# Performance work log

Measured on AMD Instinct MI355X. Metric: run time of the kernel, lower is better.

## Reference

```python
import jax, jax.numpy as jnp
import numpy as np

N, T, H, W, C = 4, 8, 64, 64, 512
WS = 8  # window size; H, W are exact multiples so pad/depad are identity


def setup_inputs() -> dict:
    key = jax.random.key(0)
    k1, k2, k3, k4 = jax.random.split(key, 4)
    x = jax.random.normal(k1, (N, T, H, W, C), dtype=jnp.float32)
    local_pos_embed = jax.random.normal(k2, (WS, WS, C), dtype=jnp.float32)
    W_in = jax.random.normal(k3, (3 * C, C), dtype=jnp.float32) * 0.02
    b_in = jnp.zeros((3 * C,), dtype=jnp.float32)
    W_out = jax.random.normal(k4, (C, C), dtype=jnp.float32) * 0.02
    b_out = jnp.zeros((C,), dtype=jnp.float32)
    return {"x": x, "local_pos_embed": local_pos_embed, "W_in": W_in,
            "b_in": b_in, "W_out": W_out, "b_out": b_out, "num_heads": 8}


def reference(x, local_pos_embed, W_in, b_in, W_out, b_out, num_heads):
    n, t, h, w, c = x.shape
    ws = local_pos_embed.shape[0]
    nh, nw = h // ws, w // ws
    head_dim = c // num_heads
    scale = 1.0 / jnp.sqrt(jnp.asarray(head_dim, dtype=x.dtype))

    # window partition: (N*T, H, W, C) -> (N*T*nh*nw, ws*ws, C)
    xw = x.reshape(n * t, nh, ws, nw, ws, c)
    xw = xw.transpose(0, 1, 3, 2, 4, 5).reshape(n * t * nh * nw, ws * ws, c)

    pos = local_pos_embed.reshape(ws * ws, c)  # flatten(0,1)
    qk_in = xw + pos[None, :, :]               # pos added to q,k only

    Wq, Wk, Wv = W_in[:c], W_in[c:2 * c], W_in[2 * c:]
    bq, bk, bv = b_in[:c], b_in[c:2 * c], b_in[2 * c:]

    B, S = qk_in.shape[0], qk_in.shape[1]
    q = (qk_in @ Wq.T + bq).reshape(B, S, num_heads, head_dim)
    k = (qk_in @ Wk.T + bk).reshape(B, S, num_heads, head_dim)
    v = (xw @ Wv.T + bv).reshape(B, S, num_heads, head_dim)

    scores = jnp.einsum('bqhd,bkhd->bhqk', q * scale, k)
    attn = jax.nn.softmax(scores, axis=-1)
    out = jnp.einsum('bhqk,bkhd->bqhd', attn, v).reshape(B, S, c)
    out = out @ W_out.T + b_out

    # reverse window partition
    out = out.reshape(n * t, nh, nw, ws, ws, c)
    out = out.transpose(0, 1, 3, 2, 4, 5).reshape(n, t, h, w, c)
    return out
```

## Files before the change

### kernel.cpp

```cpp
#include <hip/hip_runtime.h>

typedef _Float16 f16;
typedef unsigned int u32;
typedef f16 f16x8 __attribute__((ext_vector_type(8)));
typedef f16 f16x4 __attribute__((ext_vector_type(4)));
typedef float f32x4 __attribute__((ext_vector_type(4)));


__device__ __forceinline__ int src_row(int m) {
    int win = m >> 6, s = m & 63;
    return ((win >> 6) << 12) | (((win >> 3) & 7) << 9) | ((s >> 3) << 6) |
           ((win & 7) << 3) | (s & 7);
}

__device__ __forceinline__ void gload_lds16(const void* g, void* lds) {
    __builtin_amdgcn_global_load_lds(
        (const __attribute__((address_space(1))) u32*)g,
        (__attribute__((address_space(3))) u32*)lds, 16, 0, 0);
}

__global__ __launch_bounds__(256) void prep_weights_k(
        const float* __restrict__ Wi, const float* __restrict__ Wo,
        f16* __restrict__ Wi_h, f16* __restrict__ Wo_h) {
    int i = blockIdx.x * 256 + threadIdx.x;
    const float4* src;
    f16* dst;
    int idx;
    if (i < 196608) { src = (const float4*)Wi; dst = Wi_h; idx = i; }
    else            { src = (const float4*)Wo; dst = Wo_h; idx = i - 196608; }
    float4 v = src[idx];
    f16x4 h = {(f16)v.x, (f16)v.y, (f16)v.z, (f16)v.w};
    *(f16x4*)(dst + (size_t)idx * 4) = h;
}

__global__ __launch_bounds__(256) void prep_bias_k(
        const float* __restrict__ pos, const float* __restrict__ Wi,
        const float* __restrict__ b_in, float* __restrict__ biasT) {
    int idx = blockIdx.x * 256 + threadIdx.x;
    int s = idx / 1536, o = idx % 1536;
    float acc = b_in[o];
    if (o < 1024) {
        const float4* p4 = (const float4*)(pos + (size_t)s * 512);
        const float4* w4 = (const float4*)(Wi + (size_t)o * 512);
        #pragma unroll 4
        for (int c = 0; c < 128; ++c) {
            float4 a = p4[c], b = w4[c];
            acc += a.x * b.x + a.y * b.y + a.z * b.z + a.w * b.w;
        }
    }
    biasT[idx] = acc;
}

__global__ __launch_bounds__(256) void prep_x_k(
        const float* __restrict__ x, f16* __restrict__ xh, int m0) {
    int i = blockIdx.x * 256 + threadIdx.x;
    int ml = i >> 6, c8 = (i & 63) * 8;
    int sr = src_row(m0 + ml);
    const float4* s4 = (const float4*)(x + (size_t)sr * 512 + c8);
    float4 a = s4[0], b = s4[1];
    f16x8 hv = {(f16)a.x, (f16)a.y, (f16)a.z, (f16)a.w,
                (f16)b.x, (f16)b.y, (f16)b.z, (f16)b.w};
    *(f16x8*)(xh + (size_t)ml * 512 + c8) = hv;
}

__global__ void __launch_bounds__(512, 2) qkv_gemm8_k(
        const f16* __restrict__ xh, const f16* __restrict__ Wh,
        const float* __restrict__ biasT, f16* __restrict__ qk,
        f16* __restrict__ vT, int nblk) {
    extern __shared__ f16 lds[];
    int tid = threadIdx.x;
    int lane = tid & 63, wid = tid >> 6;
    int l15 = lane & 15, g = lane >> 4;
    int wm = wid >> 2, wn = wid & 3;
    int sid = (blockIdx.x & 7) * (nblk >> 3) + (blockIdx.x >> 3);
    int bm = sid / 6, bn = sid % 6;
    const f16* Ap = xh + (size_t)bm * 256 * 512;
    const f16* Bp = Wh + (size_t)bn * 256 * 512;

    int li0 = tid, li1 = tid + 512;
    int r0 = li0 >> 3, c0 = li0 & 7, r1 = li1 >> 3, c1 = li1 & 7;
    int off0 = r0 * 512 + ((c0 ^ (r0 & 7)) * 8);
    int off1 = r1 * 512 + ((c1 ^ (r1 & 7)) * 8);

    auto stage = [&](const f16* panel, int ldsbase, int tt, int h) {
        int tb = tt & 1;
        int dst = ldsbase + (tb * 2 + h) * 8192 + wid * 512;
        const f16* src = panel + h * 65536 + tt * 64;
        gload_lds16(src + off0, (void*)&lds[dst]);
        gload_lds16(src + off1, (void*)&lds[dst + 4096]);
    };

    f32x4 acc[8][4];
    f32x4 zero4 = {0.f, 0.f, 0.f, 0.f};
    #pragma unroll
    for (int a = 0; a < 8; ++a)
        #pragma unroll
        for (int b = 0; b < 4; ++b) acc[a][b] = zero4;
    f16x8 bf[4][2];

    stage(Ap, 0, 0, 0); stage(Ap, 0, 0, 1);
    stage(Bp, 32768, 0, 0); stage(Bp, 32768, 0, 1);
    stage(Ap, 0, 1, 0); stage(Ap, 0, 1, 1);
    stage(Bp, 32768, 1, 0); stage(Bp, 32768, 1, 1);
    asm volatile("s_waitcnt vmcnt(8)" ::: "memory");
    __builtin_amdgcn_s_barrier();

    #pragma unroll
    for (int tt = 0; tt < 8; ++tt) {
        int tb = tt & 1;
        const f16* Ab = &lds[(tb * 2 + wm) * 8192];
        const f16* Bb = &lds[32768 + (tb * 2 + (wn >> 1)) * 8192];
        #pragma unroll
        for (int q = 0; q < 4; ++q) {
            f16x8 af[2][2];
            #pragma unroll
            for (int ml = 0; ml < 2; ++ml) {
                int rr = (q * 2 + ml) * 16 + l15;
                #pragma unroll
                for (int ks = 0; ks < 2; ++ks)
                    af[ml][ks] = *(const f16x8*)&Ab[rr * 64 + (((ks * 4 + g) ^ (rr & 7)) * 8)];
            }
            if (q == 0) {
                #pragma unroll
                for (int nf = 0; nf < 4; ++nf) {
                    int rb = (wn & 1) * 64 + nf * 16 + l15;
                    #pragma unroll
                    for (int ks = 0; ks < 2; ++ks)
                        bf[nf][ks] = *(const f16x8*)&Bb[rb * 64 + (((ks * 4 + g) ^ (rb & 7)) * 8)];
                }
            }
            if (q <= 1) {
                if ((tt & 1) ? (tt + 1 < 8) : (tt >= 2)) stage(Ap, 0, tt + 1, q);
            } else {
                if (tt + 2 < 8) stage(Bp, 32768, tt + 2, q - 2);
            }
            __builtin_amdgcn_s_barrier();
            __builtin_amdgcn_s_setprio(1);
            #pragma unroll
            for (int ml = 0; ml < 2; ++ml)
                #pragma unroll
                for (int nf = 0; nf < 4; ++nf)
                    #pragma unroll
                    for (int ks = 0; ks < 2; ++ks)
                        acc[q * 2 + ml][nf] = __builtin_amdgcn_mfma_f32_16x16x32_f16(
                            af[ml][ks], bf[nf][ks], acc[q * 2 + ml][nf], 0, 0, 0);
            __builtin_amdgcn_s_setprio(0);
            if (q == 3) {
                if (tt < 6)       asm volatile("s_waitcnt vmcnt(4)" ::: "memory");
                else if (tt == 6) asm volatile("s_waitcnt vmcnt(0)" ::: "memory");
            }
            __builtin_amdgcn_s_barrier();
        }
    }

    int browg = bm * 256 + wm * 128;
    if (bn < 4) {
        #pragma unroll
        for (int half = 0; half < 2; ++half) {
            if (wm == half) {
                #pragma unroll
                for (int mf = 0; mf < 8; ++mf) {
                    #pragma unroll
                    for (int nf = 0; nf < 4; ++nf) {
                        int col = bn * 256 + wn * 64 + nf * 16 + l15;
                        int cloc = wn * 64 + nf * 16 + l15;
                        #pragma unroll
                        for (int j = 0; j < 4; ++j) {
                            int r = mf * 16 + g * 4 + j;
                            float v = acc[mf][nf][j] + biasT[(r & 63) * 1536 + col];
                            *(f16*)((char*)lds + r * 512 + ((cloc * 2) ^ ((r & 7) << 4))) = (f16)v;
                        }
                    }
                }
            }
            __syncthreads();
            int rowg0 = bm * 256 + half * 128;
            #pragma unroll
            for (int i = 0; i < 8; ++i) {
                int c = i * 512 + tid;
                int r = c >> 5, seg = c & 31;
                f16x8 v = *(const f16x8*)((char*)lds + r * 512 + ((seg * 16) ^ ((r & 7) << 4)));
                *(f16x8*)(qk + (size_t)(rowg0 + r) * 1024 + bn * 256 + seg * 8) = v;
            }
            __syncthreads();
        }
    } else {
        __syncthreads();
        char* T = (char*)lds;
        int bn2 = bn - 4;
        #pragma unroll
        for (int mf = 0; mf < 8; ++mf) {
            #pragma unroll
            for (int nf = 0; nf < 4; ++nf) {
                int dl = wn * 64 + nf * 16 + l15;
                float bo = biasT[1024 + bn2 * 256 + dl];
                #pragma unroll
                for (int j = 0; j < 4; ++j) {
                    int sl = wm * 128 + mf * 16 + g * 4 + j;
                    *(f16*)(T + dl * 512 + ((sl * 2) ^ ((dl & 7) << 4))) =
                        (f16)(acc[mf][nf][j] + bo);
                }
            }
        }
        __syncthreads();
        #pragma unroll
        for (int r = 0; r < 16; ++r) {
            int c = r * 512 + tid;
            int dl = c >> 5, s0 = (c & 31) * 8;
            f16x8 v = *(const f16x8*)(T + dl * 512 + ((s0 * 2) ^ ((dl & 7) << 4)));
            int gcol = bn2 * 256 + dl;
            int head = gcol >> 6, dd = gcol & 63;
            int win = bm * 4 + (s0 >> 6);
            *(f16x8*)(vT + (size_t)win * 32768 + head * 4096 + dd * 64 + (s0 & 63)) = v;
        }
    }
}

__global__ __launch_bounds__(512) void attn_k(
        const f16* __restrict__ qk, const f16* __restrict__ vT,
        f16* __restrict__ attn_h) {
    __shared__ __align__(16) char S[64 * 1024];
    int tid = threadIdx.x;
    int lane = tid & 63, h = tid >> 6;
    int l15 = lane & 15, g = lane >> 4;
    const f16* baseqk = qk + (size_t)blockIdx.x * 65536;
    const f16* basev  = vT + (size_t)blockIdx.x * 32768 + h * 4096;
    int qc = h * 64, kc = 512 + h * 64;

    f32x4 zero4 = {0.f, 0.f, 0.f, 0.f};
    f32x4 acc[4][4];
    #pragma unroll
    for (int a = 0; a < 4; ++a)
        #pragma unroll
        for (int b = 0; b < 4; ++b) acc[a][b] = zero4;

    {
        f16x8 qf[4][2], kf[4][2];
        #pragma unroll
        for (int mf = 0; mf < 4; ++mf)
            #pragma unroll
            for (int ks = 0; ks < 2; ++ks)
                qf[mf][ks] = *reinterpret_cast<const f16x8*>(baseqk + (size_t)(mf * 16 + l15) * 1024 + qc + ks * 32 + g * 8);
        #pragma unroll
        for (int nf = 0; nf < 4; ++nf)
            #pragma unroll
            for (int ks = 0; ks < 2; ++ks)
                kf[nf][ks] = *reinterpret_cast<const f16x8*>(baseqk + (size_t)(nf * 16 + l15) * 1024 + kc + ks * 32 + g * 8);
        #pragma unroll
        for (int ks = 0; ks < 2; ++ks)
            #pragma unroll
            for (int ki = 0; ki < 4; ++ki)
                #pragma unroll
                for (int qi = 0; qi < 4; ++qi)
                    acc[ki][qi] = __builtin_amdgcn_mfma_f32_16x16x32_f16(kf[ki][ks], qf[qi][ks], acc[ki][qi], 0, 0, 0);
    }

    f16x8 vf[4][2];
    #pragma unroll
    for (int nf = 0; nf < 4; ++nf)
        #pragma unroll
        for (int ks = 0; ks < 2; ++ks)
            vf[nf][ks] = *reinterpret_cast<const f16x8*>(basev + (nf * 16 + l15) * 64 + ks * 32 + g * 8);

    char* Sh = S + h * 8192;
    #pragma unroll
    for (int qi = 0; qi < 4; ++qi) {
        float mx = -1e30f;
        #pragma unroll
        for (int ki = 0; ki < 4; ++ki)
            #pragma unroll
            for (int j = 0; j < 4; ++j) mx = fmaxf(mx, acc[ki][qi][j]);
        mx = fmaxf(mx, __shfl_xor(mx, 16));
        mx = fmaxf(mx, __shfl_xor(mx, 32));
        float sum = 0.f;
        #pragma unroll
        for (int ki = 0; ki < 4; ++ki)
            #pragma unroll
            for (int j = 0; j < 4; ++j) {
                float e = __expf((acc[ki][qi][j] - mx) * 0.125f);
                acc[ki][qi][j] = e;
                sum += e;
            }
        sum += __shfl_xor(sum, 16);
        sum += __shfl_xor(sum, 32);
        float rinv = __fdividef(1.0f, sum);
        int qrow = qi * 16 + l15;
        char* rowp = Sh + qrow * 128;
        int sw = (qrow & 7) << 4;
        #pragma unroll
        for (int ki = 0; ki < 4; ++ki)
            #pragma unroll
            for (int j = 0; j < 4; ++j)
                *(f16*)(rowp + (((ki * 16 + g * 4 + j) * 2) ^ sw)) = (f16)(acc[ki][qi][j] * rinv);
    }

    f32x4 acc2[4][4];
    #pragma unroll
    for (int a = 0; a < 4; ++a)
        #pragma unroll
        for (int b = 0; b < 4; ++b) acc2[a][b] = zero4;
    #pragma unroll
    for (int ks = 0; ks < 2; ++ks)
        #pragma unroll
        for (int mf = 0; mf < 4; ++mf) {
            int rr = mf * 16 + l15;
            f16x8 pa = *reinterpret_cast<const f16x8*>(Sh + rr * 128 + (((ks * 32 + g * 8) * 2) ^ ((rr & 7) << 4)));
            #pragma unroll
            for (int nf = 0; nf < 4; ++nf)
                acc2[mf][nf] = __builtin_amdgcn_mfma_f32_16x16x32_f16(pa, vf[nf][ks], acc2[mf][nf], 0, 0, 0);
        }

    #pragma unroll
    for (int mf = 0; mf < 4; ++mf)
        #pragma unroll
        for (int nf = 0; nf < 4; ++nf)
            #pragma unroll
            for (int j = 0; j < 4; ++j) {
                int r = mf * 16 + g * 4 + j;
                *(f16*)(Sh + r * 128 + (((nf * 16 + l15) * 2) ^ ((r & 7) << 4))) = (f16)acc2[mf][nf][j];
            }
    __syncthreads();
    f16* dst = attn_h + (size_t)blockIdx.x * 32768;
    #pragma unroll
    for (int i = 0; i < 8; ++i) {
        int c = i * 512 + tid;
        int row = c >> 6, seg = c & 63;
        f16x8 v = *(const f16x8*)(S + (seg >> 3) * 8192 + row * 128 + (((seg & 7) * 16) ^ ((row & 7) << 4)));
        *(f16x8*)(dst + row * 512 + seg * 8) = v;
    }
}

__global__ void __launch_bounds__(512, 2) proj_gemm8_k(
        const f16* __restrict__ attn_h, const f16* __restrict__ Woh,
        const float* __restrict__ b_out, float* __restrict__ out, int nblk, int m0) {
    extern __shared__ f16 lds[];
    int tid = threadIdx.x;
    int lane = tid & 63, wid = tid >> 6;
    int l15 = lane & 15, g = lane >> 4;
    int wm = wid >> 2, wn = wid & 3;
    int sid = (blockIdx.x & 7) * (nblk >> 3) + (blockIdx.x >> 3);
    int bm = sid >> 1, bn = sid & 1;
    const f16* Ap = attn_h + (size_t)bm * 256 * 512;
    const f16* Bp = Woh + (size_t)bn * 256 * 512;

    int li0 = tid, li1 = tid + 512;
    int r0 = li0 >> 3, c0 = li0 & 7, r1 = li1 >> 3, c1 = li1 & 7;
    int off0 = r0 * 512 + ((c0 ^ (r0 & 7)) * 8);
    int off1 = r1 * 512 + ((c1 ^ (r1 & 7)) * 8);

    auto stage = [&](const f16* panel, int ldsbase, int tt, int h) {
        int tb = tt & 1;
        int dst = ldsbase + (tb * 2 + h) * 8192 + wid * 512;
        const f16* src = panel + h * 65536 + tt * 64;
        gload_lds16(src + off0, (void*)&lds[dst]);
        gload_lds16(src + off1, (void*)&lds[dst + 4096]);
    };

    f32x4 acc[8][4];
    f32x4 zero4 = {0.f, 0.f, 0.f, 0.f};
    #pragma unroll
    for (int a = 0; a < 8; ++a)
        #pragma unroll
        for (int b = 0; b < 4; ++b) acc[a][b] = zero4;
    f16x8 bf[4][2];

    stage(Ap, 0, 0, 0); stage(Ap, 0, 0, 1);
    stage(Bp, 32768, 0, 0); stage(Bp, 32768, 0, 1);
    stage(Ap, 0, 1, 0); stage(Ap, 0, 1, 1);
    stage(Bp, 32768, 1, 0); stage(Bp, 32768, 1, 1);
    asm volatile("s_waitcnt vmcnt(8)" ::: "memory");
    __builtin_amdgcn_s_barrier();

    #pragma unroll
    for (int tt = 0; tt < 8; ++tt) {
        int tb = tt & 1;
        const f16* Ab = &lds[(tb * 2 + wm) * 8192];
        const f16* Bb = &lds[32768 + (tb * 2 + (wn >> 1)) * 8192];
        #pragma unroll
        for (int q = 0; q < 4; ++q) {
            f16x8 af[2][2];
            #pragma unroll
            for (int ml = 0; ml < 2; ++ml) {
                int rr = (q * 2 + ml) * 16 + l15;
                #pragma unroll
                for (int ks = 0; ks < 2; ++ks)
                    af[ml][ks] = *(const f16x8*)&Ab[rr * 64 + (((ks * 4 + g) ^ (rr & 7)) * 8)];
            }
            if (q == 0) {
                #pragma unroll
                for (int nf = 0; nf < 4; ++nf) {
                    int rb = (wn & 1) * 64 + nf * 16 + l15;
                    #pragma unroll
                    for (int ks = 0; ks < 2; ++ks)
                        bf[nf][ks] = *(const f16x8*)&Bb[rb * 64 + (((ks * 4 + g) ^ (rb & 7)) * 8)];
                }
            }
            if (q <= 1) {
                if ((tt & 1) ? (tt + 1 < 8) : (tt >= 2)) stage(Ap, 0, tt + 1, q);
            } else {
                if (tt + 2 < 8) stage(Bp, 32768, tt + 2, q - 2);
            }
            __builtin_amdgcn_s_barrier();
            __builtin_amdgcn_s_setprio(1);
            #pragma unroll
            for (int ml = 0; ml < 2; ++ml)
                #pragma unroll
                for (int nf = 0; nf < 4; ++nf)
                    #pragma unroll
                    for (int ks = 0; ks < 2; ++ks)
                        acc[q * 2 + ml][nf] = __builtin_amdgcn_mfma_f32_16x16x32_f16(
                            af[ml][ks], bf[nf][ks], acc[q * 2 + ml][nf], 0, 0, 0);
            __builtin_amdgcn_s_setprio(0);
            if (q == 3) {
                if (tt < 6)       asm volatile("s_waitcnt vmcnt(4)" ::: "memory");
                else if (tt == 6) asm volatile("s_waitcnt vmcnt(0)" ::: "memory");
            }
            __builtin_amdgcn_s_barrier();
        }
    }

    int browg = bm * 256 + wm * 128, bcolg = bn * 256 + wn * 64;
    #pragma unroll
    for (int nf = 0; nf < 4; ++nf) {
        int col = bcolg + nf * 16 + l15;
        float bo = b_out[col];
        #pragma unroll
        for (int mf = 0; mf < 8; ++mf) {
            #pragma unroll
            for (int j = 0; j < 4; ++j) {
                int srow = src_row(m0 + browg + mf * 16 + g * 4 + j);
                out[(size_t)srow * 512 + col] = acc[mf][nf][j] + bo;
            }
        }
    }
}

extern "C" void kernel_launch(void* const* d_in, const int* in_sizes, int n_in,
                              void* d_out, int out_size, void* d_ws, size_t ws_size,
                              hipStream_t stream) {
    (void)in_sizes; (void)n_in; (void)out_size;
    const float* x     = (const float*)d_in[0];
    const float* pos   = (const float*)d_in[1];
    const float* W_in  = (const float*)d_in[2];
    const float* b_in  = (const float*)d_in[3];
    const float* W_out = (const float*)d_in[4];
    const float* b_out = (const float*)d_in[5];
    float* out = (float*)d_out;

    char* ws = (char*)d_ws;
    f16*   Wi_h  = (f16*)ws;
    f16*   Wo_h  = (f16*)(ws + 1572864);
    float* biasT = (float*)(ws + 2097152);
    const size_t fixed = 2490368;

    int chunks = 1;
    while (chunks < 64) {
        size_t need = fixed + ((size_t)131072 / chunks) * 4096;
        if (need <= ws_size) break;
        chunks <<= 1;
    }
    int Mc = 131072 / chunks;
    f16* xh = (f16*)(ws + fixed);
    f16* qk = (f16*)(ws + fixed + (size_t)Mc * 1024);
    f16* vT = (f16*)(ws + fixed + (size_t)Mc * 3072);
    int nblk  = (Mc / 256) * 6;
    int nblk2 = (Mc / 256) * 2;

    static_cast<void>(hipFuncSetAttribute((const void*)qkv_gemm8_k,
        hipFuncAttributeMaxDynamicSharedMemorySize, 131072));
    static_cast<void>(hipFuncSetAttribute((const void*)proj_gemm8_k,
        hipFuncAttributeMaxDynamicSharedMemorySize, 131072));

    prep_weights_k<<<1024, 256, 0, stream>>>(W_in, W_out, Wi_h, Wo_h);
    prep_bias_k<<<384, 256, 0, stream>>>(pos, W_in, b_in, biasT);
    for (int c = 0; c < chunks; ++c) {
        int m0 = c * Mc;
        prep_x_k<<<Mc / 4, 256, 0, stream>>>(x, xh, m0);
        qkv_gemm8_k<<<nblk, 512, 131072, stream>>>(xh, Wi_h, biasT, qk, vT, nblk);
        attn_k<<<Mc / 64, 512, 0, stream>>>(qk, vT, xh);
        proj_gemm8_k<<<nblk2, 512, 131072, stream>>>(xh, Wo_h, b_out, out, nblk2, m0);
    }
}
```

Measured before the change: 603.4 us.

## Make GEMM blocks process four M tiles with a continuous cross-tile prefetch pipeline

Both the QKV and projection GEMM kernels now handle four consecutive 256-row tiles per block, keeping the LDS prefetch pipeline running across tile boundaries instead of refilling it for each tile. This amortises prologue and epilogue latency and cuts the grid to a quarter of its previous size. The QKV epilogue also drops its LDS-staged transpose and writes q/k and vT straight to global memory with scalar or 4-wide stores. In exchange the grid may be too small to fill all CUs, and the direct stores are less coalesced than the staged 16-byte ones.

```diff
diff --git a/kernel.cpp b/kernel.cpp
--- a/kernel.cpp
+++ b/kernel.cpp
@@ -73,8 +73,8 @@
     int l15 = lane & 15, g = lane >> 4;
     int wm = wid >> 2, wn = wid & 3;
     int sid = (blockIdx.x & 7) * (nblk >> 3) + (blockIdx.x >> 3);
-    int bm = sid / 6, bn = sid % 6;
-    const f16* Ap = xh + (size_t)bm * 256 * 512;
+    int bmg = sid / 6, bn = sid % 6;
+    const f16* Ap = xh + (size_t)bmg * 4 * 256 * 512;
     const f16* Bp = Wh + (size_t)bn * 256 * 512;
 
     int li0 = tid, li1 = tid + 512;
@@ -82,13 +82,18 @@
     int off0 = r0 * 512 + ((c0 ^ (r0 & 7)) * 8);
     int off1 = r1 * 512 + ((c1 ^ (r1 & 7)) * 8);
 
-    auto stage = [&](const f16* panel, int ldsbase, int tt, int h) {
-        int tb = tt & 1;
-        int dst = ldsbase + (tb * 2 + h) * 8192 + wid * 512;
-        const f16* src = panel + h * 65536 + tt * 64;
+    auto stageA = [&](int Tabs, int h) {
+        int dst = ((Tabs & 1) * 2 + h) * 8192 + wid * 512;
+        const f16* src = Ap + (size_t)(Tabs >> 3) * 131072 + h * 65536 + (Tabs & 7) * 64;
         gload_lds16(src + off0, (void*)&lds[dst]);
         gload_lds16(src + off1, (void*)&lds[dst + 4096]);
     };
+    auto stageB = [&](int Tabs, int h) {
+        int dst = 32768 + ((Tabs & 1) * 2 + h) * 8192 + wid * 512;
+        const f16* src = Bp + h * 65536 + (Tabs & 7) * 64;
+        gload_lds16(src + off0, (void*)&lds[dst]);
+        gload_lds16(src + off1, (void*)&lds[dst + 4096]);
+    };
 
     f32x4 acc[8][4];
     f32x4 zero4 = {0.f, 0.f, 0.f, 0.f};
@@ -98,121 +103,103 @@
         for (int b = 0; b < 4; ++b) acc[a][b] = zero4;
     f16x8 bf[4][2];
 
-    stage(Ap, 0, 0, 0); stage(Ap, 0, 0, 1);
-    stage(Bp, 32768, 0, 0); stage(Bp, 32768, 0, 1);
-    stage(Ap, 0, 1, 0); stage(Ap, 0, 1, 1);
-    stage(Bp, 32768, 1, 0); stage(Bp, 32768, 1, 1);
+    stageA(0, 0); stageA(0, 1); stageB(0, 0); stageB(0, 1);
+    stageA(1, 0); stageA(1, 1); stageB(1, 0); stageB(1, 1);
     asm volatile("s_waitcnt vmcnt(8)" ::: "memory");
     __builtin_amdgcn_s_barrier();
 
-    #pragma unroll
-    for (int tt = 0; tt < 8; ++tt) {
-        int tb = tt & 1;
-        const f16* Ab = &lds[(tb * 2 + wm) * 8192];
-        const f16* Bb = &lds[32768 + (tb * 2 + (wn >> 1)) * 8192];
-        #pragma unroll
-        for (int q = 0; q < 4; ++q) {
-            f16x8 af[2][2];
-            #pragma unroll
-            for (int ml = 0; ml < 2; ++ml) {
-                int rr = (q * 2 + ml) * 16 + l15;
-                #pragma unroll
-                for (int ks = 0; ks < 2; ++ks)
-                    af[ml][ks] = *(const f16x8*)&Ab[rr * 64 + (((ks * 4 + g) ^ (rr & 7)) * 8)];
-            }
-            if (q == 0) {
+    for (int p = 0; p < 4; ++p) {
+        #pragma unroll
+        for (int tt = 0; tt < 8; ++tt) {
+            const f16* Ab = &lds[((tt & 1) * 2 + wm) * 8192];
+            const f16* Bb = &lds[32768 + ((tt & 1) * 2 + (wn >> 1)) * 8192];
+            #pragma unroll
+            for (int q = 0; q < 4; ++q) {
+                f16x8 af[2][2];
+                #pragma unroll
+                for (int ml = 0; ml < 2; ++ml) {
+                    int rr = (q * 2 + ml) * 16 + l15;
+                    #pragma unroll
+                    for (int ks = 0; ks < 2; ++ks)
+                        af[ml][ks] = *(const f16x8*)&Ab[rr * 64 + (((ks * 4 + g) ^ (rr & 7)) * 8)];
+                }
+                if (q == 0) {
+                    #pragma unroll
+                    for (int nf = 0; nf < 4; ++nf) {
+                        int rb = (wn & 1) * 64 + nf * 16 + l15;
+                        #pragma unroll
+                        for (int ks = 0; ks < 2; ++ks)
+                            bf[nf][ks] = *(const f16x8*)&Bb[rb * 64 + (((ks * 4 + g) ^ (rb & 7)) * 8)];
+                    }
+                }
+                if (q <= 1) {
+                    bool doA = (tt >= 1 || p > 0) && (tt < 7 || p < 3);
+                    if (doA) stageA(p * 8 + tt + 1, q);
+                } else {
+                    bool doB = (tt < 6 || p < 3);
+                    if (doB) stageB(p * 8 + tt + 2, q - 2);
+                }
+                __builtin_amdgcn_s_barrier();
+                __builtin_amdgcn_s_setprio(1);
+                #pragma unroll
+                for (int ml = 0; ml < 2; ++ml)
+                    #pragma unroll
+                    for (int nf = 0; nf < 4; ++nf)
+                        #pragma unroll
+                        for (int ks = 0; ks < 2; ++ks)
+                            acc[q * 2 + ml][nf] = __builtin_amdgcn_mfma_f32_16x16x32_f16(
+                                af[ml][ks], bf[nf][ks], acc[q * 2 + ml][nf], 0, 0, 0);
+                __builtin_amdgcn_s_setprio(0);
+                if (q == 3) {
+                    if (tt < 6) {
+                        asm volatile("s_waitcnt vmcnt(4)" ::: "memory");
+                    } else if (tt == 6) {
+                        if (p < 3) asm volatile("s_waitcnt vmcnt(4)" ::: "memory");
+                        else       asm volatile("s_waitcnt vmcnt(0)" ::: "memory");
+                    } else {
+                        if (p < 3) asm volatile("s_waitcnt vmcnt(4)" ::: "memory");
+                    }
+                }
+                __builtin_amdgcn_s_barrier();
+            }
+        }
+
+        int browg = (bmg * 4 + p) * 256 + wm * 128;
+        if (bn < 4) {
+            #pragma unroll
+            for (int mf = 0; mf < 8; ++mf) {
                 #pragma unroll
                 for (int nf = 0; nf < 4; ++nf) {
-                    int rb = (wn & 1) * 64 + nf * 16 + l15;
-                    #pragma unroll
-                    for (int ks = 0; ks < 2; ++ks)
-                        bf[nf][ks] = *(const f16x8*)&Bb[rb * 64 + (((ks * 4 + g) ^ (rb & 7)) * 8)];
-                }
-            }
-            if (q <= 1) {
-                if ((tt & 1) ? (tt + 1 < 8) : (tt >= 2)) stage(Ap, 0, tt + 1, q);
-            } else {
-                if (tt + 2 < 8) stage(Bp, 32768, tt + 2, q - 2);
-            }
-            __builtin_amdgcn_s_barrier();
-            __builtin_amdgcn_s_setprio(1);
-            #pragma unroll
-            for (int ml = 0; ml < 2; ++ml)
-                #pragma unroll
-                for (int nf = 0; nf < 4; ++nf)
-                    #pragma unroll
-                    for (int ks = 0; ks < 2; ++ks)
-                        acc[q * 2 + ml][nf] = __builtin_amdgcn_mfma_f32_16x16x32_f16(
-                            af[ml][ks], bf[nf][ks], acc[q * 2 + ml][nf], 0, 0, 0);
-            __builtin_amdgcn_s_setprio(0);
-            if (q == 3) {
-                if (tt < 6)       asm volatile("s_waitcnt vmcnt(4)" ::: "memory");
-                else if (tt == 6) asm volatile("s_waitcnt vmcnt(0)" ::: "memory");
-            }
-            __builtin_amdgcn_s_barrier();
-        }
-    }
-
-    int browg = bm * 256 + wm * 128;
-    if (bn < 4) {
-        #pragma unroll
-        for (int half = 0; half < 2; ++half) {
-            if (wm == half) {
-                #pragma unroll
-                for (int mf = 0; mf < 8; ++mf) {
-                    #pragma unroll
-                    for (int nf = 0; nf < 4; ++nf) {
-                        int col = bn * 256 + wn * 64 + nf * 16 + l15;
-                        int cloc = wn * 64 + nf * 16 + l15;
-                        #pragma unroll
-                        for (int j = 0; j < 4; ++j) {
-                            int r = mf * 16 + g * 4 + j;
-                            float v = acc[mf][nf][j] + biasT[(r & 63) * 1536 + col];
-                            *(f16*)((char*)lds + r * 512 + ((cloc * 2) ^ ((r & 7) << 4))) = (f16)v;
-                        }
+                    int col = bn * 256 + wn * 64 + nf * 16 + l15;
+                    #pragma unroll
+                    for (int j = 0; j < 4; ++j) {
+                        int row = browg + mf * 16 + g * 4 + j;
+                        float v = acc[mf][nf][j] + biasT[(row & 63) * 1536 + col];
+                        qk[(size_t)row * 1024 + col] = (f16)v;
                     }
                 }
             }
-            __syncthreads();
-            int rowg0 = bm * 256 + half * 128;
-            #pragma unroll
-            for (int i = 0; i < 8; ++i) {
-                int c = i * 512 + tid;
-                int r = c >> 5, seg = c & 31;
-                f16x8 v = *(const f16x8*)((char*)lds + r * 512 + ((seg * 16) ^ ((r & 7) << 4)));
-                *(f16x8*)(qk + (size_t)(rowg0 + r) * 1024 + bn * 256 + seg * 8) = v;
-            }
-            __syncthreads();
-        }
-    } else {
-        __syncthreads();
-        char* T = (char*)lds;
-        int bn2 = bn - 4;
-        #pragma unroll
-        for (int mf = 0; mf < 8; ++mf) {
-            #pragma unroll
-            for (int nf = 0; nf < 4; ++nf) {
-                int dl = wn * 64 + nf * 16 + l15;
-                float bo = biasT[1024 + bn2 * 256 + dl];
-                #pragma unroll
-                for (int j = 0; j < 4; ++j) {
-                    int sl = wm * 128 + mf * 16 + g * 4 + j;
-                    *(f16*)(T + dl * 512 + ((sl * 2) ^ ((dl & 7) << 4))) =
-                        (f16)(acc[mf][nf][j] + bo);
-                }
-            }
-        }
-        __syncthreads();
-        #pragma unroll
-        for (int r = 0; r < 16; ++r) {
-            int c = r * 512 + tid;
-            int dl = c >> 5, s0 = (c & 31) * 8;
-            f16x8 v = *(const f16x8*)(T + dl * 512 + ((s0 * 2) ^ ((dl & 7) << 4)));
-            int gcol = bn2 * 256 + dl;
-            int head = gcol >> 6, dd = gcol & 63;
-            int win = bm * 4 + (s0 >> 6);
-            *(f16x8*)(vT + (size_t)win * 32768 + head * 4096 + dd * 64 + (s0 & 63)) = v;
-        }
+        } else {
+            int bn2 = bn - 4;
+            #pragma unroll
+            for (int mf = 0; mf < 8; ++mf) {
+                int sl = browg + mf * 16 + g * 4;
+                int win = sl >> 6, s = sl & 63;
+                #pragma unroll
+                for (int nf = 0; nf < 4; ++nf) {
+                    int dl = bn2 * 256 + wn * 64 + nf * 16 + l15;
+                    float bo = biasT[1024 + dl];
+                    int head = dl >> 6, dd = dl & 63;
+                    f16x4 v = {(f16)(acc[mf][nf][0] + bo), (f16)(acc[mf][nf][1] + bo),
+                               (f16)(acc[mf][nf][2] + bo), (f16)(acc[mf][nf][3] + bo)};
+                    *(f16x4*)(vT + (size_t)win * 32768 + head * 4096 + dd * 64 + s) = v;
+                }
+            }
+        }
+        #pragma unroll
+        for (int a = 0; a < 8; ++a)
+            #pragma unroll
+            for (int b = 0; b < 4; ++b) acc[a][b] = zero4;
     }
 }
 
@@ -339,8 +326,8 @@
     int l15 = lane & 15, g = lane >> 4;
     int wm = wid >> 2, wn = wid & 3;
     int sid = (blockIdx.x & 7) * (nblk >> 3) + (blockIdx.x >> 3);
-    int bm = sid >> 1, bn = sid & 1;
-    const f16* Ap = attn_h + (size_t)bm * 256 * 512;
+    int bmg = sid >> 1, bn = sid & 1;
+    const f16* Ap = attn_h + (size_t)bmg * 4 * 256 * 512;
     const f16* Bp = Woh + (size_t)bn * 256 * 512;
 
     int li0 = tid, li1 = tid + 512;
@@ -348,13 +335,18 @@
     int off0 = r0 * 512 + ((c0 ^ (r0 & 7)) * 8);
     int off1 = r1 * 512 + ((c1 ^ (r1 & 7)) * 8);
 
-    auto stage = [&](const f16* panel, int ldsbase, int tt, int h) {
-        int tb = tt & 1;
-        int dst = ldsbase + (tb * 2 + h) * 8192 + wid * 512;
-        const f16* src = panel + h * 65536 + tt * 64;
+    auto stageA = [&](int Tabs, int h) {
+        int dst = ((Tabs & 1) * 2 + h) * 8192 + wid * 512;
+        const f16* src = Ap + (size_t)(Tabs >> 3) * 131072 + h * 65536 + (Tabs & 7) * 64;
         gload_lds16(src + off0, (void*)&lds[dst]);
         gload_lds16(src + off1, (void*)&lds[dst + 4096]);
     };
+    auto stageB = [&](int Tabs, int h) {
+        int dst = 32768 + ((Tabs & 1) * 2 + h) * 8192 + wid * 512;
+        const f16* src = Bp + h * 65536 + (Tabs & 7) * 64;
+        gload_lds16(src + off0, (void*)&lds[dst]);
+        gload_lds16(src + off1, (void*)&lds[dst + 4096]);
+    };
 
     f32x4 acc[8][4];
     f32x4 zero4 = {0.f, 0.f, 0.f, 0.f};
@@ -364,74 +356,86 @@
         for (int b = 0; b < 4; ++b) acc[a][b] = zero4;
     f16x8 bf[4][2];
 
-    stage(Ap, 0, 0, 0); stage(Ap, 0, 0, 1);
-    stage(Bp, 32768, 0, 0); stage(Bp, 32768, 0, 1);
-    stage(Ap, 0, 1, 0); stage(Ap, 0, 1, 1);
-    stage(Bp, 32768, 1, 0); stage(Bp, 32768, 1, 1);
+    stageA(0, 0); stageA(0, 1); stageB(0, 0); stageB(0, 1);
+    stageA(1, 0); stageA(1, 1); stageB(1, 0); stageB(1, 1);
     asm volatile("s_waitcnt vmcnt(8)" ::: "memory");
     __builtin_amdgcn_s_barrier();
 
-    #pragma unroll
-    for (int tt = 0; tt < 8; ++tt) {
-        int tb = tt & 1;
-        const f16* Ab = &lds[(tb * 2 + wm) * 8192];
-        const f16* Bb = &lds[32768 + (tb * 2 + (wn >> 1)) * 8192];
-        #pragma unroll
-        for (int q = 0; q < 4; ++q) {
-            f16x8 af[2][2];
-            #pragma unroll
-            for (int ml = 0; ml < 2; ++ml) {
-                int rr = (q * 2 + ml) * 16 + l15;
-                #pragma unroll
-                for (int ks = 0; ks < 2; ++ks)
-                    af[ml][ks] = *(const f16x8*)&Ab[rr * 64 + (((ks * 4 + g) ^ (rr & 7)) * 8)];
-            }
-            if (q == 0) {
-                #pragma unroll
-                for (int nf = 0; nf < 4; ++nf) {
-                    int rb = (wn & 1) * 64 + nf * 16 + l15;
+    for (int p = 0; p < 4; ++p) {
+        #pragma unroll
+        for (int tt = 0; tt < 8; ++tt) {
+            const f16* Ab = &lds[((tt & 1) * 2 + wm) * 8192];
+            const f16* Bb = &lds[32768 + ((tt & 1) * 2 + (wn >> 1)) * 8192];
+            #pragma unroll
+            for (int q = 0; q < 4; ++q) {
+                f16x8 af[2][2];
+                #pragma unroll
+                for (int ml = 0; ml < 2; ++ml) {
+                    int rr = (q * 2 + ml) * 16 + l15;
                     #pragma unroll
                     for (int ks = 0; ks < 2; ++ks)
-                        bf[nf][ks] = *(const f16x8*)&Bb[rb * 64 + (((ks * 4 + g) ^ (rb & 7)) * 8)];
-                }
-            }
-            if (q <= 1) {
-                if ((tt & 1) ? (tt + 1 < 8) : (tt >= 2)) stage(Ap, 0, tt + 1, q);
-            } else {
-                if (tt + 2 < 8) stage(Bp, 32768, tt + 2, q - 2);
-            }
-            __builtin_amdgcn_s_barrier();
-            __builtin_amdgcn_s_setprio(1);
-            #pragma unroll
-            for (int ml = 0; ml < 2; ++ml)
-                #pragma unroll
-                for (int nf = 0; nf < 4; ++nf)
-                    #pragma unroll
-                    for (int ks = 0; ks < 2; ++ks)
-                        acc[q * 2 + ml][nf] = __builtin_amdgcn_mfma_f32_16x16x32_f16(
-                            af[ml][ks], bf[nf][ks], acc[q * 2 + ml][nf], 0, 0, 0);
-            __builtin_amdgcn_s_setprio(0);
-            if (q == 3) {
-                if (tt < 6)       asm volatile("s_waitcnt vmcnt(4)" ::: "memory");
-                else if (tt == 6) asm volatile("s_waitcnt vmcnt(0)" ::: "memory");
-            }
-            __builtin_amdgcn_s_barrier();
-        }
-    }
-
-    int browg = bm * 256 + wm * 128, bcolg = bn * 256 + wn * 64;
-    #pragma unroll
-    for (int nf = 0; nf < 4; ++nf) {
-        int col = bcolg + nf * 16 + l15;
-        float bo = b_out[col];
-        #pragma unroll
-        for (int mf = 0; mf < 8; ++mf) {
-            #pragma unroll
-            for (int j = 0; j < 4; ++j) {
-                int srow = src_row(m0 + browg + mf * 16 + g * 4 + j);
-                out[(size_t)srow * 512 + col] = acc[mf][nf][j] + bo;
-            }
-        }
+                        af[ml][ks] = *(const f16x8*)&Ab[rr * 64 + (((ks * 4 + g) ^ (rr & 7)) * 8)];
+                }
+                if (q == 0) {
+                    #pragma unroll
+                    for (int nf = 0; nf < 4; ++nf) {
+                        int rb = (wn & 1) * 64 + nf * 16 + l15;
+                        #pragma unroll
+                        for (int ks = 0; ks < 2; ++ks)
+                            bf[nf][ks] = *(const f16x8*)&Bb[rb * 64 + (((ks * 4 + g) ^ (rb & 7)) * 8)];
+                    }
+                }
+                if (q <= 1) {
+                    bool doA = (tt >= 1 || p > 0) && (tt < 7 || p < 3);
+                    if (doA) stageA(p * 8 + tt + 1, q);
+                } else {
+                    bool doB = (tt < 6 || p < 3);
+                    if (doB) stageB(p * 8 + tt + 2, q - 2);
+                }
+                __builtin_amdgcn_s_barrier();
+                __builtin_amdgcn_s_setprio(1);
+                #pragma unroll
+                for (int ml = 0; ml < 2; ++ml)
+                    #pragma unroll
+                    for (int nf = 0; nf < 4; ++nf)
+                        #pragma unroll
+                        for (int ks = 0; ks < 2; ++ks)
+                            acc[q * 2 + ml][nf] = __builtin_amdgcn_mfma_f32_16x16x32_f16(
+                                af[ml][ks], bf[nf][ks], acc[q * 2 + ml][nf], 0, 0, 0);
+                __builtin_amdgcn_s_setprio(0);
+                if (q == 3) {
+                    if (tt < 6) {
+                        asm volatile("s_waitcnt vmcnt(4)" ::: "memory");
+                    } else if (tt == 6) {
+                        if (p < 3) asm volatile("s_waitcnt vmcnt(4)" ::: "memory");
+                        else       asm volatile("s_waitcnt vmcnt(0)" ::: "memory");
+                    } else {
+                        if (p < 3) asm volatile("s_waitcnt vmcnt(4)" ::: "memory");
+                    }
+                }
+                __builtin_amdgcn_s_barrier();
+            }
+        }
+
+        int browg = (bmg * 4 + p) * 256 + wm * 128;
+        int bcolg = bn * 256 + wn * 64;
+        #pragma unroll
+        for (int nf = 0; nf < 4; ++nf) {
+            int col = bcolg + nf * 16 + l15;
+            float bo = b_out[col];
+            #pragma unroll
+            for (int mf = 0; mf < 8; ++mf) {
+                #pragma unroll
+                for (int j = 0; j < 4; ++j) {
+                    int srow = src_row(m0 + browg + mf * 16 + g * 4 + j);
+                    out[(size_t)srow * 512 + col] = acc[mf][nf][j] + bo;
+                }
+            }
+        }
+        #pragma unroll
+        for (int a = 0; a < 8; ++a)
+            #pragma unroll
+            for (int b = 0; b < 4; ++b) acc[a][b] = zero4;
     }
 }
 
@@ -463,8 +467,8 @@
     f16* xh = (f16*)(ws + fixed);
     f16* qk = (f16*)(ws + fixed + (size_t)Mc * 1024);
     f16* vT = (f16*)(ws + fixed + (size_t)Mc * 3072);
-    int nblk  = (Mc / 256) * 6;
-    int nblk2 = (Mc / 256) * 2;
+    int nblk  = (Mc / 1024) * 6;
+    int nblk2 = (Mc / 1024) * 2;
 
     static_cast<void>(hipFuncSetAttribute((const void*)qkv_gemm8_k,
         hipFuncAttributeMaxDynamicSharedMemorySize, 131072));
```

After: 1.121 ms. 1.86x slower.

## Split attention blocks per half-heads, drop LDS staging in QK epilogue, chunk by four

Applied to the files above, without the earlier changes.

The attention kernel is split into two 256-thread blocks per window, each handling four heads. Each block uses 16KB of LDS and processes the probability matrix in two K-halves, which lowers LDS and register pressure to allow more resident blocks. Attention results and the Q/K epilogue of the QKV GEMM are now written straight to global memory with scattered 2-byte stores instead of being staged through LDS for coalesced 16-byte stores. The minimum chunk count rises to 4, which shrinks the workspace footprint, possibly for L2/MALL locality, but adds more kernel launches.

```diff
diff --git a/kernel.cpp b/kernel.cpp
--- a/kernel.cpp
+++ b/kernel.cpp
@@ -156,33 +156,17 @@
     int browg = bm * 256 + wm * 128;
     if (bn < 4) {
         #pragma unroll
-        for (int half = 0; half < 2; ++half) {
-            if (wm == half) {
-                #pragma unroll
-                for (int mf = 0; mf < 8; ++mf) {
-                    #pragma unroll
-                    for (int nf = 0; nf < 4; ++nf) {
-                        int col = bn * 256 + wn * 64 + nf * 16 + l15;
-                        int cloc = wn * 64 + nf * 16 + l15;
-                        #pragma unroll
-                        for (int j = 0; j < 4; ++j) {
-                            int r = mf * 16 + g * 4 + j;
-                            float v = acc[mf][nf][j] + biasT[(r & 63) * 1536 + col];
-                            *(f16*)((char*)lds + r * 512 + ((cloc * 2) ^ ((r & 7) << 4))) = (f16)v;
-                        }
-                    }
+        for (int mf = 0; mf < 8; ++mf) {
+            #pragma unroll
+            for (int nf = 0; nf < 4; ++nf) {
+                int col = bn * 256 + wn * 64 + nf * 16 + l15;
+                #pragma unroll
+                for (int j = 0; j < 4; ++j) {
+                    int row = browg + mf * 16 + g * 4 + j;
+                    float v = acc[mf][nf][j] + biasT[(row & 63) * 1536 + col];
+                    qk[(size_t)row * 1024 + col] = (f16)v;
                 }
             }
-            __syncthreads();
-            int rowg0 = bm * 256 + half * 128;
-            #pragma unroll
-            for (int i = 0; i < 8; ++i) {
-                int c = i * 512 + tid;
-                int r = c >> 5, seg = c & 31;
-                f16x8 v = *(const f16x8*)((char*)lds + r * 512 + ((seg * 16) ^ ((r & 7) << 4)));
-                *(f16x8*)(qk + (size_t)(rowg0 + r) * 1024 + bn * 256 + seg * 8) = v;
-            }
-            __syncthreads();
         }
     } else {
         __syncthreads();
@@ -216,16 +200,18 @@
     }
 }
 
-__global__ __launch_bounds__(512) void attn_k(
+__global__ __launch_bounds__(256, 6) void attn_k(
         const f16* __restrict__ qk, const f16* __restrict__ vT,
         f16* __restrict__ attn_h) {
-    __shared__ __align__(16) char S[64 * 1024];
+    __shared__ __align__(16) char S[16 * 1024];
     int tid = threadIdx.x;
-    int lane = tid & 63, h = tid >> 6;
+    int lane = tid & 63, w = tid >> 6;
     int l15 = lane & 15, g = lane >> 4;
-    const f16* baseqk = qk + (size_t)blockIdx.x * 65536;
-    const f16* basev  = vT + (size_t)blockIdx.x * 32768 + h * 4096;
-    int qc = h * 64, kc = 512 + h * 64;
+    int win = blockIdx.x >> 1;
+    int head = (blockIdx.x & 1) * 4 + w;
+    const f16* baseqk = qk + (size_t)win * 65536;
+    const f16* basev  = vT + (size_t)win * 32768 + head * 4096;
+    int qc = head * 64, kc = 512 + head * 64;
 
     f32x4 zero4 = {0.f, 0.f, 0.f, 0.f};
     f32x4 acc[4][4];
@@ -255,14 +241,6 @@
                     acc[ki][qi] = __builtin_amdgcn_mfma_f32_16x16x32_f16(kf[ki][ks], qf[qi][ks], acc[ki][qi], 0, 0, 0);
     }
 
-    f16x8 vf[4][2];
-    #pragma unroll
-    for (int nf = 0; nf < 4; ++nf)
-        #pragma unroll
-        for (int ks = 0; ks < 2; ++ks)
-            vf[nf][ks] = *reinterpret_cast<const f16x8*>(basev + (nf * 16 + l15) * 64 + ks * 32 + g * 8);
-
-    char* Sh = S + h * 8192;
     #pragma unroll
     for (int qi = 0; qi < 4; ++qi) {
         float mx = -1e30f;
@@ -284,50 +262,58 @@
         sum += __shfl_xor(sum, 16);
         sum += __shfl_xor(sum, 32);
         float rinv = __fdividef(1.0f, sum);
-        int qrow = qi * 16 + l15;
-        char* rowp = Sh + qrow * 128;
-        int sw = (qrow & 7) << 4;
         #pragma unroll
         for (int ki = 0; ki < 4; ++ki)
             #pragma unroll
+            for (int j = 0; j < 4; ++j) acc[ki][qi][j] *= rinv;
+    }
+
+    char* Sh = S + w * 4096;
+    f32x4 acc2[4][4];
+    #pragma unroll
+    for (int a = 0; a < 4; ++a)
+        #pragma unroll
+        for (int b = 0; b < 4; ++b) acc2[a][b] = zero4;
+
+    #pragma unroll
+    for (int hf = 0; hf < 2; ++hf) {
+        #pragma unroll
+        for (int k2 = 0; k2 < 2; ++k2) {
+            int ki = hf * 2 + k2;
+            #pragma unroll
+            for (int qi = 0; qi < 4; ++qi) {
+                int row = qi * 16 + l15;
+                char* rowp = Sh + row * 64;
+                #pragma unroll
+                for (int j = 0; j < 4; ++j) {
+                    int kl = k2 * 16 + g * 4 + j;
+                    *(f16*)(rowp + ((((kl >> 3) ^ (row & 3)) << 4) | ((kl & 7) * 2))) =
+                        (f16)acc[ki][qi][j];
+                }
+            }
+        }
+        f16x8 vfh[4];
+        #pragma unroll
+        for (int nf = 0; nf < 4; ++nf)
+            vfh[nf] = *reinterpret_cast<const f16x8*>(basev + (nf * 16 + l15) * 64 + hf * 32 + g * 8);
+        #pragma unroll
+        for (int mf = 0; mf < 4; ++mf) {
+            int row = mf * 16 + l15;
+            f16x8 pa = *reinterpret_cast<const f16x8*>(Sh + row * 64 + ((g ^ (row & 3)) << 4));
+            #pragma unroll
+            for (int nf = 0; nf < 4; ++nf)
+                acc2[mf][nf] = __builtin_amdgcn_mfma_f32_16x16x32_f16(pa, vfh[nf], acc2[mf][nf], 0, 0, 0);
+        }
+    }
+
+    f16* dst = attn_h + (size_t)win * 32768 + head * 64;
+    #pragma unroll
+    for (int mf = 0; mf < 4; ++mf)
+        #pragma unroll
+        for (int nf = 0; nf < 4; ++nf)
+            #pragma unroll
             for (int j = 0; j < 4; ++j)
-                *(f16*)(rowp + (((ki * 16 + g * 4 + j) * 2) ^ sw)) = (f16)(acc[ki][qi][j] * rinv);
-    }
-
-    f32x4 acc2[4][4];
-    #pragma unroll
-    for (int a = 0; a < 4; ++a)
-        #pragma unroll
-        for (int b = 0; b < 4; ++b) acc2[a][b] = zero4;
-    #pragma unroll
-    for (int ks = 0; ks < 2; ++ks)
-        #pragma unroll
-        for (int mf = 0; mf < 4; ++mf) {
-            int rr = mf * 16 + l15;
-            f16x8 pa = *reinterpret_cast<const f16x8*>(Sh + rr * 128 + (((ks * 32 + g * 8) * 2) ^ ((rr & 7) << 4)));
-            #pragma unroll
-            for (int nf = 0; nf < 4; ++nf)
-                acc2[mf][nf] = __builtin_amdgcn_mfma_f32_16x16x32_f16(pa, vf[nf][ks], acc2[mf][nf], 0, 0, 0);
-        }
-
-    #pragma unroll
-    for (int mf = 0; mf < 4; ++mf)
-        #pragma unroll
-        for (int nf = 0; nf < 4; ++nf)
-            #pragma unroll
-            for (int j = 0; j < 4; ++j) {
-                int r = mf * 16 + g * 4 + j;
-                *(f16*)(Sh + r * 128 + (((nf * 16 + l15) * 2) ^ ((r & 7) << 4))) = (f16)acc2[mf][nf][j];
-            }
-    __syncthreads();
-    f16* dst = attn_h + (size_t)blockIdx.x * 32768;
-    #pragma unroll
-    for (int i = 0; i < 8; ++i) {
-        int c = i * 512 + tid;
-        int row = c >> 6, seg = c & 63;
-        f16x8 v = *(const f16x8*)(S + (seg >> 3) * 8192 + row * 128 + (((seg & 7) * 16) ^ ((row & 7) << 4)));
-        *(f16x8*)(dst + row * 512 + seg * 8) = v;
-    }
+                dst[(size_t)(mf * 16 + g * 4 + j) * 512 + nf * 16 + l15] = (f16)acc2[mf][nf][j];
 }
 
 __global__ void __launch_bounds__(512, 2) proj_gemm8_k(
@@ -453,7 +439,7 @@
     float* biasT = (float*)(ws + 2097152);
     const size_t fixed = 2490368;
 
-    int chunks = 1;
+    int chunks = 4;
     while (chunks < 64) {
         size_t need = fixed + ((size_t)131072 / chunks) * 4096;
         if (need <= ws_size) break;
@@ -464,7 +450,7 @@
     f16* qk = (f16*)(ws + fixed + (size_t)Mc * 1024);
     f16* vT = (f16*)(ws + fixed + (size_t)Mc * 3072);
     int nblk  = (Mc / 256) * 6;
-    int nblk2 = (Mc / 256) * 2;
+    int nblkP = (Mc / 256) * 2;
 
     static_cast<void>(hipFuncSetAttribute((const void*)qkv_gemm8_k,
         hipFuncAttributeMaxDynamicSharedMemorySize, 131072));
@@ -477,7 +463,7 @@
         int m0 = c * Mc;
         prep_x_k<<<Mc / 4, 256, 0, stream>>>(x, xh, m0);
         qkv_gemm8_k<<<nblk, 512, 131072, stream>>>(xh, Wi_h, biasT, qk, vT, nblk);
-        attn_k<<<Mc / 64, 512, 0, stream>>>(qk, vT, xh);
-        proj_gemm8_k<<<nblk2, 512, 131072, stream>>>(xh, Wo_h, b_out, out, nblk2, m0);
-    }
-}
+        attn_k<<<(Mc / 64) * 2, 256, 0, stream>>>(qk, vT, xh);
+        proj_gemm8_k<<<nblkP, 512, 131072, stream>>>(xh, Wo_h, b_out, out, nblkP, m0);
+    }
+}
```

Result: slower. 798.7 us (+32.4%).
